# Kernel tuning notes

Hardware: AMD Instinct MI355X
Metric: run time of the kernel (lower is better)

The kernel has to match this reference:

```python
import jax, jax.numpy as jnp
import numpy as np

N_NODES = 50000
N_EDGES = 800000
IN_DIM = 128
HID = 64
HEADS = 4
OUT_DIM = 128
NEG_SLOPE = 0.2


def setup_inputs() -> dict:
    key = jax.random.key(0)
    ks = jax.random.split(key, 11)
    x = jax.random.normal(ks[0], (N_NODES, IN_DIM), dtype=jnp.float32)
    edge_index = jax.random.randint(ks[1], (2, N_EDGES), 0, N_NODES, dtype=jnp.int64)
    s1 = 1.0 / np.sqrt(IN_DIM)
    s2 = 1.0 / np.sqrt(HEADS * HID)
    W1 = jax.random.normal(ks[2], (IN_DIM, HEADS * HID), dtype=jnp.float32) * s1
    a_src1 = jax.random.normal(ks[3], (HEADS, HID), dtype=jnp.float32) * s2
    a_dst1 = jax.random.normal(ks[4], (HEADS, HID), dtype=jnp.float32) * s2
    b1 = jnp.zeros((HEADS * HID,), dtype=jnp.float32)
    W2 = jax.random.normal(ks[5], (HEADS * HID, OUT_DIM), dtype=jnp.float32) * s2
    a_src2 = jax.random.normal(ks[6], (1, OUT_DIM), dtype=jnp.float32) * 0.1
    a_dst2 = jax.random.normal(ks[7], (1, OUT_DIM), dtype=jnp.float32) * 0.1
    b2 = jnp.zeros((OUT_DIM,), dtype=jnp.float32)
    return {"x": x, "edge_index": edge_index, "W1": W1, "a_src1": a_src1,
            "a_dst1": a_dst1, "b1": b1, "W2": W2, "a_src2": a_src2,
            "a_dst2": a_dst2, "b2": b2}


def _gat_conv(x, src, dst, W, a_src, a_dst, bias, heads, out_per_head, concat):
    n = x.shape[0]
    # linear projection per head: [N, H, F]
    h = (x @ W).reshape(n, heads, out_per_head)
    # per-node attention terms: [N, H]
    alpha_src = jnp.einsum('nhf,hf->nh', h, a_src)
    alpha_dst = jnp.einsum('nhf,hf->nh', h, a_dst)
    # edge logits with LeakyReLU: [E, H]
    e = jax.nn.leaky_relu(alpha_src[src] + alpha_dst[dst], NEG_SLOPE)
    # softmax over incoming edges of each destination node
    m = jax.ops.segment_max(e, dst, num_segments=n)  # [N, H]
    m = jnp.where(jnp.isfinite(m), m, 0.0)
    e = jnp.exp(e - m[dst])
    denom = jax.ops.segment_sum(e, dst, num_segments=n)  # [N, H]
    alpha = e / (denom[dst] + 1e-16)  # [E, H]
    # weighted scatter-aggregate of source messages
    out = jax.ops.segment_sum(h[src] * alpha[:, :, None], dst, num_segments=n)  # [N, H, F]
    if concat:
        out = out.reshape(n, heads * out_per_head)
    else:
        out = out.mean(axis=1)
    return out + bias


def reference(x, edge_index, W1, a_src1, a_dst1, b1, W2, a_src2, a_dst2, b2):
    n = x.shape[0]
    # PyG GATConv adds self-loops by default
    loops = jnp.arange(n, dtype=edge_index.dtype)
    src = jnp.concatenate([edge_index[0], loops])
    dst = jnp.concatenate([edge_index[1], loops])
    # dropout layers are identity in inference
    h = _gat_conv(x, src, dst, W1, a_src1, a_dst1, b1, HEADS, HID, True)
    h = jax.nn.elu(h)
    out = _gat_conv(h, src, dst, W2, a_src2, a_dst2, b2, 1, OUT_DIM, True)
    # F.normalize(p=2, dim=1)
    norm = jnp.linalg.norm(out, axis=1, keepdims=True)
    return out / jnp.maximum(norm, 1e-12)
```

## Files before the change

### kernel.cpp

```cpp
#include <hip/hip_runtime.h>
#include <hip/hip_fp16.h>
#include <math.h>

#define N_NODES 50000
#define N_EDGES 800000
#define ET (N_EDGES + N_NODES)
#define IN_DIM 128
#define HID 64
#define HEADS 4
#define C1 (HEADS * HID)
#define OUT_DIM 128
#define NEG_SLOPE 0.2f
#define MTILES 3125
#define G1GRP 782
#define SCB 977
#define SCAN_B 1024
#define NSCB 49
#define HB 64
#define EPB (N_EDGES / HB)

typedef _Float16 h8 __attribute__((ext_vector_type(8)));
typedef float f4 __attribute__((ext_vector_type(4)));
typedef unsigned short u16;

__device__ __forceinline__ float leaky(float v) { return fmaxf(v, NEG_SLOPE * v); }
__device__ __forceinline__ float elu(float v) { return v > 0.0f ? v : expm1f(v); }

__device__ __forceinline__ void fma_mix8(float* acc, h8 v, float w) {
    union { h8 h; int i[4]; } u; u.h = v;
#pragma unroll
    for (int k = 0; k < 4; ++k) {
        asm("v_fma_mix_f32 %0, %1, %2, %0 op_sel:[0,0,0] op_sel_hi:[1,0,0]"
            : "+v"(acc[2 * k]) : "v"(u.i[k]), "v"(w));
        asm("v_fma_mix_f32 %0, %1, %2, %0 op_sel:[1,0,0] op_sel_hi:[1,0,0]"
            : "+v"(acc[2 * k + 1]) : "v"(u.i[k]), "v"(w));
    }
}

__global__ __launch_bounds__(256) void hist_kernel(
        const float* __restrict__ W1, const float* __restrict__ W2,
        __half* __restrict__ w1t, __half* __restrict__ w2t,
        const int* __restrict__ dst, u16* __restrict__ cnt_mat,
        u16* __restrict__ lrank16) {
    __shared__ unsigned pk[N_NODES / 4];
    const int b = blockIdx.x, t = threadIdx.x;
    for (int i = b * 256 + t; i < IN_DIM * C1; i += HB * 256) {
        int k1 = i >> 8, n1 = i & 255;
        w1t[n1 * IN_DIM + k1] = __float2half(W1[i]);
        int k2 = i >> 7, n2 = i & 127;
        w2t[n2 * C1 + k2] = __float2half(W2[i]);
    }
    const int e0 = b * EPB;
    const int4* d4p = (const int4*)(dst + e0);
#pragma unroll
    for (int half = 0; half < 2; ++half) {
        const int nbase = half * (N_NODES / 2);
        for (int i = t; i < N_NODES / 4; i += 256) pk[i] = 0;
        __syncthreads();
        for (int k4 = t; k4 < EPB / 4; k4 += 256) {
            int4 d4 = d4p[k4];
            int dd0 = d4.x - nbase, dd1 = d4.y - nbase;
            int dd2 = d4.z - nbase, dd3 = d4.w - nbase;
            if ((unsigned)dd0 < (unsigned)(N_NODES / 2)) {
                unsigned r = atomicAdd(&pk[dd0 >> 1], (dd0 & 1) ? 65536u : 1u);
                lrank16[e0 + k4 * 4 + 0] = (u16)((dd0 & 1) ? (r >> 16) : (r & 0xffffu));
            }
            if ((unsigned)dd1 < (unsigned)(N_NODES / 2)) {
                unsigned r = atomicAdd(&pk[dd1 >> 1], (dd1 & 1) ? 65536u : 1u);
                lrank16[e0 + k4 * 4 + 1] = (u16)((dd1 & 1) ? (r >> 16) : (r & 0xffffu));
            }
            if ((unsigned)dd2 < (unsigned)(N_NODES / 2)) {
                unsigned r = atomicAdd(&pk[dd2 >> 1], (dd2 & 1) ? 65536u : 1u);
                lrank16[e0 + k4 * 4 + 2] = (u16)((dd2 & 1) ? (r >> 16) : (r & 0xffffu));
            }
            if ((unsigned)dd3 < (unsigned)(N_NODES / 2)) {
                unsigned r = atomicAdd(&pk[dd3 >> 1], (dd3 & 1) ? 65536u : 1u);
                lrank16[e0 + k4 * 4 + 3] = (u16)((dd3 & 1) ? (r >> 16) : (r & 0xffffu));
            }
        }
        __syncthreads();
        unsigned* crow = (unsigned*)(cnt_mat + (size_t)b * N_NODES) + half * (N_NODES / 4);
        for (int i = t; i < N_NODES / 4; i += 256) crow[i] = pk[i];
        __syncthreads();
    }
}

__global__ void scan_local(const u16* __restrict__ cnt_mat, u16* __restrict__ boff,
                           int* __restrict__ lscan, int* __restrict__ bsum) {
    __shared__ int wsum[16];
    const int t = threadIdx.x, lane = t & 63, wv = t >> 6;
    int idx = blockIdx.x * SCAN_B + t;
    int run = 0;
    if (idx < N_NODES) {
#pragma unroll 8
        for (int b = 0; b < HB; ++b) {
            u16 c = cnt_mat[(size_t)b * N_NODES + idx];
            boff[(size_t)b * N_NODES + idx] = (u16)run;
            run += c;
        }
    }
    int v = (idx < N_NODES) ? run + 1 : 0;
    int sc = v;
#pragma unroll
    for (int o = 1; o < 64; o <<= 1) {
        int u = __shfl_up(sc, o);
        if (lane >= o) sc += u;
    }
    if (lane == 63) wsum[wv] = sc;
    __syncthreads();
    if (t == 0) {
        int run2 = 0;
#pragma unroll
        for (int w = 0; w < 16; ++w) { int s = wsum[w]; wsum[w] = run2; run2 += s; }
        bsum[blockIdx.x] = run2;
    }
    __syncthreads();
    if (idx < N_NODES) lscan[idx] = sc + wsum[wv];
}

__global__ void scan_final(const int* __restrict__ lscan, const int* __restrict__ bsum,
                           int* __restrict__ rp) {
    __shared__ int base;
    if (threadIdx.x == 0) {
        int s = 0;
        for (int b = 0; b < blockIdx.x; ++b) s += bsum[b];
        base = s;
    }
    __syncthreads();
    int idx = blockIdx.x * SCAN_B + threadIdx.x;
    if (idx == 0) rp[0] = 0;
    if (idx >= N_NODES) return;
    rp[idx + 1] = lscan[idx] + base;
}

__global__ __launch_bounds__(256) void gemm1_scatter(
        const float* __restrict__ x, const __half* __restrict__ w1t,
        const float* __restrict__ aws, const float* __restrict__ awd,
        __half* __restrict__ hpm, float* __restrict__ as1m, float* __restrict__ ad1m,
        const int* __restrict__ src, const int* __restrict__ dst,
        const u16* __restrict__ lrank16, const u16* __restrict__ boff,
        const int* __restrict__ rp, u16* __restrict__ cs16) {
    const int q9 = blockIdx.x / 9, r9 = blockIdx.x % 9;
    if (r9 >= 4) {
        int si = q9 * 5 + (r9 - 4);
        int tid = si * 256 + threadIdx.x;
        if (tid < N_EDGES / 4) {
            const int b = tid / (EPB / 4);
            const u16* bo = boff + (size_t)b * N_NODES;
            int4 s4 = ((const int4*)src)[tid];
            int4 d4 = ((const int4*)dst)[tid];
            ushort4 r4 = ((const ushort4*)lrank16)[tid];
            cs16[rp[d4.x] + (int)bo[d4.x] + (int)r4.x] = (u16)s4.x;
            cs16[rp[d4.y] + (int)bo[d4.y] + (int)r4.y] = (u16)s4.y;
            cs16[rp[d4.z] + (int)bo[d4.z] + (int)r4.z] = (u16)s4.z;
            cs16[rp[d4.w] + (int)bo[d4.w] + (int)r4.w] = (u16)s4.w;
        } else {
            int d = tid - N_EDGES / 4;
            if (d < N_NODES) cs16[rp[d + 1] - 1] = (u16)d;
        }
        return;
    }
    const int g = q9 * 4 + r9;
    const int tile = g * 4 + (threadIdx.x >> 6);
    if (tile >= MTILES) return;
    const int lane = threadIdx.x & 63;
    const int m0 = tile * 16, lm = lane & 15, lq = lane >> 4;
    h8 afrag[4];
    const float4* xrow = (const float4*)(x + (size_t)(m0 + lm) * IN_DIM + lq * 8);
#pragma unroll
    for (int kt = 0; kt < 4; ++kt) {
        float4 a = xrow[kt * 8];
        float4 b = xrow[kt * 8 + 1];
        union { h8 v; __half2 p[4]; } u;
        u.p[0] = __floats2half2_rn(a.x, a.y);
        u.p[1] = __floats2half2_rn(a.z, a.w);
        u.p[2] = __floats2half2_rn(b.x, b.y);
        u.p[3] = __floats2half2_rn(b.z, b.w);
        afrag[kt] = u.v;
    }
    f4 acc[16];
#pragma unroll
    for (int nt = 0; nt < 16; ++nt) acc[nt] = (f4){0.f, 0.f, 0.f, 0.f};
#pragma unroll
    for (int nt = 0; nt < 16; ++nt) {
        const h8* brow = (const h8*)(w1t + (size_t)(nt * 16 + lm) * IN_DIM + lq * 8);
#pragma unroll
        for (int kt = 0; kt < 4; ++kt)
            acc[nt] = __builtin_amdgcn_mfma_f32_16x16x32_f16(afrag[kt], brow[kt * 4],
                                                             acc[nt], 0, 0, 0);
    }
    float sS[4][4] = {{0.f}}, sD[4][4] = {{0.f}};
#pragma unroll
    for (int nt = 0; nt < 16; ++nt) {
        int col = nt * 16 + lm;
        float wa = aws[col], wd = awd[col];
        int hd = nt >> 2;
        int pr = nt >> 3;
        int cip = col & 127;
#pragma unroll
        for (int r = 0; r < 4; ++r) {
            float v = acc[nt][r];
            hpm[((size_t)pr * N_NODES + (m0 + lq * 4 + r)) * 128 + cip] = __float2half(v);
            sS[hd][r] += v * wa;
            sD[hd][r] += v * wd;
        }
    }
#pragma unroll
    for (int o = 1; o < 16; o <<= 1) {
#pragma unroll
        for (int hd = 0; hd < 4; ++hd)
#pragma unroll
            for (int r = 0; r < 4; ++r) {
                sS[hd][r] += __shfl_xor(sS[hd][r], o);
                sD[hd][r] += __shfl_xor(sD[hd][r], o);
            }
    }
    if (lm == 0) {
        float2* asp = (float2*)as1m;
        float2* adp = (float2*)ad1m;
#pragma unroll
        for (int r = 0; r < 4; ++r) {
            int row = m0 + lq * 4 + r;
            asp[row]           = make_float2(sS[0][r], sS[1][r]);
            asp[N_NODES + row] = make_float2(sS[2][r], sS[3][r]);
            adp[row]           = make_float2(sD[0][r], sD[1][r]);
            adp[N_NODES + row] = make_float2(sD[2][r], sD[3][r]);
        }
    }
}

__global__ __launch_bounds__(256) void gemm2_mfma(
        const __half* __restrict__ ah, const __half* __restrict__ w2t,
        const float* __restrict__ aws, const float* __restrict__ awd,
        __half* __restrict__ h, float* __restrict__ as2, float* __restrict__ ad2) {
    const int tile = blockIdx.x * 4 + (threadIdx.x >> 6);
    if (tile >= MTILES) return;
    const int lane = threadIdx.x & 63;
    const int m0 = tile * 16, lm = lane & 15, lq = lane >> 4;
    h8 afrag[8];
    const h8* arow = (const h8*)(ah + (size_t)(m0 + lm) * C1 + lq * 8);
#pragma unroll
    for (int kt = 0; kt < 8; ++kt) afrag[kt] = arow[kt * 4];
    f4 acc[8];
#pragma unroll
    for (int nt = 0; nt < 8; ++nt) acc[nt] = (f4){0.f, 0.f, 0.f, 0.f};
#pragma unroll
    for (int nt = 0; nt < 8; ++nt) {
        const h8* brow = (const h8*)(w2t + (size_t)(nt * 16 + lm) * C1 + lq * 8);
#pragma unroll
        for (int kt = 0; kt < 8; ++kt)
            acc[nt] = __builtin_amdgcn_mfma_f32_16x16x32_f16(afrag[kt], brow[kt * 4],
                                                             acc[nt], 0, 0, 0);
    }
    float sS[4] = {0.f, 0.f, 0.f, 0.f}, sD[4] = {0.f, 0.f, 0.f, 0.f};
#pragma unroll
    for (int nt = 0; nt < 8; ++nt) {
        int col = nt * 16 + lm;
        float wa = aws[col], wd = awd[col];
#pragma unroll
        for (int r = 0; r < 4; ++r) {
            float v = acc[nt][r];
            h[(size_t)(m0 + lq * 4 + r) * OUT_DIM + col] = __float2half(v);
            sS[r] += v * wa;
            sD[r] += v * wd;
        }
    }
#pragma unroll
    for (int o = 1; o < 16; o <<= 1) {
#pragma unroll
        for (int r = 0; r < 4; ++r) {
            sS[r] += __shfl_xor(sS[r], o);
            sD[r] += __shfl_xor(sD[r], o);
        }
    }
    if (lm == 0) {
#pragma unroll
        for (int r = 0; r < 4; ++r) {
            int row = m0 + lq * 4 + r;
            as2[row] = sS[r];
            ad2[row] = sD[r];
        }
    }
}

__global__ __launch_bounds__(256) void aggregate1_fused(
        const int* __restrict__ rp, const u16* __restrict__ cs16,
        const __half* __restrict__ hpm, const float* __restrict__ as1m,
        const float* __restrict__ ad1m, const float* __restrict__ b1,
        __half* __restrict__ out1h) {
    __shared__ int4 stg[8][32];
    const int pair = blockIdx.x & 1, g = blockIdx.x >> 1;
    const int hw = threadIdx.x >> 5, li = threadIdx.x & 31;
    const int d = g * 8 + hw;
    const int e0 = rp[d], deg = rp[d + 1] - e0;
    const float2* asb = (const float2*)as1m + (size_t)pair * N_NODES;
    const float2 adv = ((const float2*)ad1m)[(size_t)pair * N_NODES + d];
    const char* hb = (const char*)hpm + (size_t)pair * N_NODES * 256;
    const int es = li >> 4, fl = li & 15;
    const int hip = fl >> 3;
    const int lbyte = fl * 16;
    float acc[8] = {0.f, 0.f, 0.f, 0.f, 0.f, 0.f, 0.f, 0.f};
    float ds0 = 0.f, ds1 = 0.f;
    for (int c0 = 0; c0 < deg; c0 += 32) {
        const int clen = min(32, deg - c0);
        int idx = c0 + li;
        bool valid = idx < deg;
        int s = valid ? (int)cs16[e0 + idx] : 0;
        float2 av = asb[s];
        float x0 = valid ? __expf(leaky(av.x + adv.x)) : 0.f;
        float x1 = valid ? __expf(leaky(av.y + adv.y)) : 0.f;
        stg[hw][li] = make_int4(s << 8, __float_as_int(x0), __float_as_int(x1), 0);
        ds0 += x0; ds1 += x1;
        __builtin_amdgcn_wave_barrier();
        int j = 0;
        for (; j + 8 <= clen; j += 8) {
            int4 p0 = stg[hw][j + es];
            int4 p1 = stg[hw][j + 2 + es];
            int4 p2 = stg[hw][j + 4 + es];
            int4 p3 = stg[hw][j + 6 + es];
            h8 v0 = *(const h8*)(hb + p0.x + lbyte);
            h8 v1 = *(const h8*)(hb + p1.x + lbyte);
            h8 v2 = *(const h8*)(hb + p2.x + lbyte);
            h8 v3 = *(const h8*)(hb + p3.x + lbyte);
            fma_mix8(acc, v0, __int_as_float(hip ? p0.z : p0.y));
            fma_mix8(acc, v1, __int_as_float(hip ? p1.z : p1.y));
            fma_mix8(acc, v2, __int_as_float(hip ? p2.z : p2.y));
            fma_mix8(acc, v3, __int_as_float(hip ? p3.z : p3.y));
        }
        for (; j < clen; j += 2) {
            int4 p0 = stg[hw][j + es];
            h8 v0 = *(const h8*)(hb + p0.x + lbyte);
            fma_mix8(acc, v0, __int_as_float(hip ? p0.z : p0.y));
        }
        __builtin_amdgcn_wave_barrier();
    }
#pragma unroll
    for (int f = 0; f < 8; ++f) acc[f] += __shfl_xor(acc[f], 16);
#pragma unroll
    for (int o = 16; o > 0; o >>= 1) {
        ds0 += __shfl_xor(ds0, o);
        ds1 += __shfl_xor(ds1, o);
    }
    if (es == 0) {
        float den = hip ? ds1 : ds0;
        float inv = 1.0f / (den + 1e-16f);
        float4 bA = ((const float4*)b1)[pair * 32 + fl * 2];
        float4 bB = ((const float4*)b1)[pair * 32 + fl * 2 + 1];
        h8 o;
        o[0] = (_Float16)elu(acc[0] * inv + bA.x);
        o[1] = (_Float16)elu(acc[1] * inv + bA.y);
        o[2] = (_Float16)elu(acc[2] * inv + bA.z);
        o[3] = (_Float16)elu(acc[3] * inv + bA.w);
        o[4] = (_Float16)elu(acc[4] * inv + bB.x);
        o[5] = (_Float16)elu(acc[5] * inv + bB.y);
        o[6] = (_Float16)elu(acc[6] * inv + bB.z);
        o[7] = (_Float16)elu(acc[7] * inv + bB.w);
        *(h8*)((char*)out1h + (size_t)d * 512 + pair * 256 + lbyte) = o;
    }
}

__global__ __launch_bounds__(256) void aggregate2_fused(
        const int* __restrict__ rp, const u16* __restrict__ cs16,
        const __half* __restrict__ h2h, const float* __restrict__ as2,
        const float* __restrict__ ad2, const float* __restrict__ b2,
        float* __restrict__ out) {
    __shared__ int2 stg[8][32];
    const int hw = threadIdx.x >> 5, li = threadIdx.x & 31;
    const int d = blockIdx.x * 8 + hw;
    const int e0 = rp[d], deg = rp[d + 1] - e0;
    const float adv = ad2[d];
    const int q = li >> 4, lo = li & 15;
    const int lbyte = lo * 16;
    const char* hbase = (const char*)h2h;
    float acc[8] = {0.f, 0.f, 0.f, 0.f, 0.f, 0.f, 0.f, 0.f};
    float dsum = 0.f;
    for (int c0 = 0; c0 < deg; c0 += 32) {
        const int clen = min(32, deg - c0);
        int idx = c0 + li;
        bool valid = idx < deg;
        int s = valid ? (int)cs16[e0 + idx] : 0;
        float xv = valid ? __expf(leaky(as2[s] + adv)) : 0.f;
        stg[hw][li] = make_int2(s << 8, __float_as_int(xv));
        dsum += xv;
        __builtin_amdgcn_wave_barrier();
        int j = 0;
        for (; j + 8 <= clen; j += 8) {
            int2 p0 = stg[hw][j + q];
            int2 p1 = stg[hw][j + 2 + q];
            int2 p2 = stg[hw][j + 4 + q];
            int2 p3 = stg[hw][j + 6 + q];
            h8 v0 = *(const h8*)(hbase + p0.x + lbyte);
            h8 v1 = *(const h8*)(hbase + p1.x + lbyte);
            h8 v2 = *(const h8*)(hbase + p2.x + lbyte);
            h8 v3 = *(const h8*)(hbase + p3.x + lbyte);
            fma_mix8(acc, v0, __int_as_float(p0.y));
            fma_mix8(acc, v1, __int_as_float(p1.y));
            fma_mix8(acc, v2, __int_as_float(p2.y));
            fma_mix8(acc, v3, __int_as_float(p3.y));
        }
        for (; j < clen; j += 2) {
            int2 p0 = stg[hw][j + q];
            h8 v0 = *(const h8*)(hbase + p0.x + lbyte);
            fma_mix8(acc, v0, __int_as_float(p0.y));
        }
        __builtin_amdgcn_wave_barrier();
    }
#pragma unroll
    for (int f = 0; f < 8; ++f) acc[f] += __shfl_xor(acc[f], 16);
#pragma unroll
    for (int o = 16; o > 0; o >>= 1) dsum += __shfl_xor(dsum, o);
    if (q == 0) {
        float inv = 1.0f / (dsum + 1e-16f);
        float4 bA = ((const float4*)b2)[lo * 2];
        float4 bB = ((const float4*)b2)[lo * 2 + 1];
        float v0 = acc[0] * inv + bA.x, v1 = acc[1] * inv + bA.y;
        float v2 = acc[2] * inv + bA.z, v3 = acc[3] * inv + bA.w;
        float v4 = acc[4] * inv + bB.x, v5 = acc[5] * inv + bB.y;
        float v6 = acc[6] * inv + bB.z, v7 = acc[7] * inv + bB.w;
        float ss = v0 * v0 + v1 * v1 + v2 * v2 + v3 * v3 +
                   v4 * v4 + v5 * v5 + v6 * v6 + v7 * v7;
#pragma unroll
        for (int o = 1; o < 16; o <<= 1) ss += __shfl_xor(ss, o);
        float sc = 1.0f / fmaxf(sqrtf(ss), 1e-12f);
        float4* orow = (float4*)((char*)out + (size_t)d * 512 + lo * 32);
        orow[0] = make_float4(v0 * sc, v1 * sc, v2 * sc, v3 * sc);
        orow[1] = make_float4(v4 * sc, v5 * sc, v6 * sc, v7 * sc);
    }
}

extern "C" void kernel_launch(void* const* d_in, const int* in_sizes, int n_in,
                              void* d_out, int out_size, void* d_ws, size_t ws_size,
                              hipStream_t stream) {
    const float* x     = (const float*)d_in[0];
    const int*   edge  = (const int*)d_in[1];
    const int*   src   = edge;
    const int*   dst   = edge + N_EDGES;
    const float* W1    = (const float*)d_in[2];
    const float* aw_s1 = (const float*)d_in[3];
    const float* aw_d1 = (const float*)d_in[4];
    const float* b1    = (const float*)d_in[5];
    const float* W2    = (const float*)d_in[6];
    const float* aw_s2 = (const float*)d_in[7];
    const float* aw_d2 = (const float*)d_in[8];
    const float* b2    = (const float*)d_in[9];
    float* out = (float*)d_out;

    char* ws = (char*)d_ws;
    size_t off = 0;
    auto alloc = [&](size_t bytes) {
        void* p = ws + off;
        off += (bytes + 255) & ~(size_t)255;
        return p;
    };
    u16*    cs16    = (u16*)alloc((size_t)ET * 2);
    u16*    lrank16 = (u16*)alloc((size_t)N_EDGES * 2);
    u16*    cnt_mat = (u16*)alloc((size_t)HB * N_NODES * 2);
    u16*    boff    = (u16*)alloc((size_t)HB * N_NODES * 2);
    int*    rp      = (int*)alloc((size_t)(N_NODES + 1) * 4);
    int*    lscan   = (int*)alloc((size_t)NSCB * SCAN_B * 4);
    int*    bsum    = (int*)alloc((size_t)NSCB * 4);
    float*  as1     = (float*)alloc((size_t)N_NODES * HEADS * 4);
    float*  ad1     = (float*)alloc((size_t)N_NODES * HEADS * 4);
    float*  as2     = (float*)alloc((size_t)N_NODES * 4);
    float*  ad2     = (float*)alloc((size_t)N_NODES * 4);
    __half* w1t     = (__half*)alloc((size_t)IN_DIM * C1 * 2);
    __half* w2t     = (__half*)alloc((size_t)C1 * OUT_DIM * 2);
    __half* hpm     = (__half*)alloc((size_t)N_NODES * C1 * 2);
    __half* out1h   = (__half*)alloc((size_t)N_NODES * C1 * 2);
    __half* h2h     = hpm;
    (void)off;


    hist_kernel<<<HB, 256, 0, stream>>>(W1, W2, w1t, w2t, dst, cnt_mat, lrank16);
    scan_local<<<NSCB, SCAN_B, 0, stream>>>(cnt_mat, boff, lscan, bsum);
    scan_final<<<NSCB, SCAN_B, 0, stream>>>(lscan, bsum, rp);
    gemm1_scatter<<<196 * 9, 256, 0, stream>>>(x, w1t, aw_s1, aw_d1, hpm, as1, ad1,
                                               src, dst, lrank16, boff, rp, cs16);

    aggregate1_fused<<<(N_NODES / 8) * 2, 256, 0, stream>>>(rp, cs16, hpm, as1, ad1, b1, out1h);

    gemm2_mfma<<<(MTILES + 3) / 4, 256, 0, stream>>>(out1h, w2t, aw_s2, aw_d2, h2h, as2, ad2);
    aggregate2_fused<<<N_NODES / 8, 256, 0, stream>>>(rp, cs16, h2h, as2, ad2, b2, out);
}
```

Baseline: 295.8 us.

## Split histogram into quarter-node blocks and split two big launches in half

The histogram kernel now runs 256 blocks, each covering one quarter of the node range, instead of 64 blocks that each loop over two halves. Each block uses a smaller shared array and needs fewer syncs, and the weight conversion loop becomes a single strided pass. The gemm1_scatter and aggregate1_fused launches are each split into two launches with a block-offset parameter. Every block still reads its full edge slice, so total dst reads per block-set grow fourfold, and the extra launches add overhead.

```diff
diff --git a/kernel.cpp b/kernel.cpp
--- a/kernel.cpp
+++ b/kernel.cpp
@@ -13,11 +13,11 @@
 #define NEG_SLOPE 0.2f
 #define MTILES 3125
 #define G1GRP 782
-#define SCB 977
 #define SCAN_B 1024
 #define NSCB 49
 #define HB 64
 #define EPB (N_EDGES / HB)
+#define NQ (N_NODES / 4)
 
 typedef _Float16 h8 __attribute__((ext_vector_type(8)));
 typedef float f4 __attribute__((ext_vector_type(4)));
@@ -42,47 +42,48 @@
         __half* __restrict__ w1t, __half* __restrict__ w2t,
         const int* __restrict__ dst, u16* __restrict__ cnt_mat,
         u16* __restrict__ lrank16) {
-    __shared__ unsigned pk[N_NODES / 4];
-    const int b = blockIdx.x, t = threadIdx.x;
-    for (int i = b * 256 + t; i < IN_DIM * C1; i += HB * 256) {
-        int k1 = i >> 8, n1 = i & 255;
-        w1t[n1 * IN_DIM + k1] = __float2half(W1[i]);
-        int k2 = i >> 7, n2 = i & 127;
-        w2t[n2 * C1 + k2] = __float2half(W2[i]);
+    __shared__ unsigned pk[NQ / 2];
+    const int b = blockIdx.x >> 2;
+    const int qd = blockIdx.x & 3;
+    const int t = threadIdx.x;
+    {
+        int i = blockIdx.x * 256 + t;
+        if (i < IN_DIM * C1) {
+            int k1 = i >> 8, n1 = i & 255;
+            w1t[n1 * IN_DIM + k1] = __float2half(W1[i]);
+            int k2 = i >> 7, n2 = i & 127;
+            w2t[n2 * C1 + k2] = __float2half(W2[i]);
+        }
     }
     const int e0 = b * EPB;
+    const int nbase = qd * NQ;
+    for (int i = t; i < NQ / 2; i += 256) pk[i] = 0;
+    __syncthreads();
     const int4* d4p = (const int4*)(dst + e0);
-#pragma unroll
-    for (int half = 0; half < 2; ++half) {
-        const int nbase = half * (N_NODES / 2);
-        for (int i = t; i < N_NODES / 4; i += 256) pk[i] = 0;
-        __syncthreads();
-        for (int k4 = t; k4 < EPB / 4; k4 += 256) {
-            int4 d4 = d4p[k4];
-            int dd0 = d4.x - nbase, dd1 = d4.y - nbase;
-            int dd2 = d4.z - nbase, dd3 = d4.w - nbase;
-            if ((unsigned)dd0 < (unsigned)(N_NODES / 2)) {
-                unsigned r = atomicAdd(&pk[dd0 >> 1], (dd0 & 1) ? 65536u : 1u);
-                lrank16[e0 + k4 * 4 + 0] = (u16)((dd0 & 1) ? (r >> 16) : (r & 0xffffu));
-            }
-            if ((unsigned)dd1 < (unsigned)(N_NODES / 2)) {
-                unsigned r = atomicAdd(&pk[dd1 >> 1], (dd1 & 1) ? 65536u : 1u);
-                lrank16[e0 + k4 * 4 + 1] = (u16)((dd1 & 1) ? (r >> 16) : (r & 0xffffu));
-            }
-            if ((unsigned)dd2 < (unsigned)(N_NODES / 2)) {
-                unsigned r = atomicAdd(&pk[dd2 >> 1], (dd2 & 1) ? 65536u : 1u);
-                lrank16[e0 + k4 * 4 + 2] = (u16)((dd2 & 1) ? (r >> 16) : (r & 0xffffu));
-            }
-            if ((unsigned)dd3 < (unsigned)(N_NODES / 2)) {
-                unsigned r = atomicAdd(&pk[dd3 >> 1], (dd3 & 1) ? 65536u : 1u);
-                lrank16[e0 + k4 * 4 + 3] = (u16)((dd3 & 1) ? (r >> 16) : (r & 0xffffu));
-            }
-        }
-        __syncthreads();
-        unsigned* crow = (unsigned*)(cnt_mat + (size_t)b * N_NODES) + half * (N_NODES / 4);
-        for (int i = t; i < N_NODES / 4; i += 256) crow[i] = pk[i];
-        __syncthreads();
-    }
+    for (int k4 = t; k4 < EPB / 4; k4 += 256) {
+        int4 d4 = d4p[k4];
+        int dd0 = d4.x - nbase, dd1 = d4.y - nbase;
+        int dd2 = d4.z - nbase, dd3 = d4.w - nbase;
+        if ((unsigned)dd0 < (unsigned)NQ) {
+            unsigned r = atomicAdd(&pk[dd0 >> 1], (dd0 & 1) ? 65536u : 1u);
+            lrank16[e0 + k4 * 4 + 0] = (u16)((dd0 & 1) ? (r >> 16) : (r & 0xffffu));
+        }
+        if ((unsigned)dd1 < (unsigned)NQ) {
+            unsigned r = atomicAdd(&pk[dd1 >> 1], (dd1 & 1) ? 65536u : 1u);
+            lrank16[e0 + k4 * 4 + 1] = (u16)((dd1 & 1) ? (r >> 16) : (r & 0xffffu));
+        }
+        if ((unsigned)dd2 < (unsigned)NQ) {
+            unsigned r = atomicAdd(&pk[dd2 >> 1], (dd2 & 1) ? 65536u : 1u);
+            lrank16[e0 + k4 * 4 + 2] = (u16)((dd2 & 1) ? (r >> 16) : (r & 0xffffu));
+        }
+        if ((unsigned)dd3 < (unsigned)NQ) {
+            unsigned r = atomicAdd(&pk[dd3 >> 1], (dd3 & 1) ? 65536u : 1u);
+            lrank16[e0 + k4 * 4 + 3] = (u16)((dd3 & 1) ? (r >> 16) : (r & 0xffffu));
+        }
+    }
+    __syncthreads();
+    unsigned* crow = (unsigned*)(cnt_mat + (size_t)b * N_NODES + nbase);
+    for (int i = t; i < NQ / 2; i += 256) crow[i] = pk[i];
 }
 
 __global__ void scan_local(const u16* __restrict__ cnt_mat, u16* __restrict__ boff,
@@ -139,8 +140,9 @@
         __half* __restrict__ hpm, float* __restrict__ as1m, float* __restrict__ ad1m,
         const int* __restrict__ src, const int* __restrict__ dst,
         const u16* __restrict__ lrank16, const u16* __restrict__ boff,
-        const int* __restrict__ rp, u16* __restrict__ cs16) {
-    const int q9 = blockIdx.x / 9, r9 = blockIdx.x % 9;
+        const int* __restrict__ rp, u16* __restrict__ cs16, int gbase) {
+    const int vb = blockIdx.x + gbase;
+    const int q9 = vb / 9, r9 = vb % 9;
     if (r9 >= 4) {
         int si = q9 * 5 + (r9 - 4);
         int tid = si * 256 + threadIdx.x;
@@ -287,9 +289,10 @@
         const int* __restrict__ rp, const u16* __restrict__ cs16,
         const __half* __restrict__ hpm, const float* __restrict__ as1m,
         const float* __restrict__ ad1m, const float* __restrict__ b1,
-        __half* __restrict__ out1h) {
+        __half* __restrict__ out1h, int gbase) {
     __shared__ int4 stg[8][32];
-    const int pair = blockIdx.x & 1, g = blockIdx.x >> 1;
+    const int vb = blockIdx.x + gbase;
+    const int pair = vb & 1, g = vb >> 1;
     const int hw = threadIdx.x >> 5, li = threadIdx.x & 31;
     const int d = g * 8 + hw;
     const int e0 = rp[d], deg = rp[d + 1] - e0;
@@ -471,13 +474,16 @@
     (void)off;
 
 
-    hist_kernel<<<HB, 256, 0, stream>>>(W1, W2, w1t, w2t, dst, cnt_mat, lrank16);
+    hist_kernel<<<HB * 4, 256, 0, stream>>>(W1, W2, w1t, w2t, dst, cnt_mat, lrank16);
     scan_local<<<NSCB, SCAN_B, 0, stream>>>(cnt_mat, boff, lscan, bsum);
     scan_final<<<NSCB, SCAN_B, 0, stream>>>(lscan, bsum, rp);
-    gemm1_scatter<<<196 * 9, 256, 0, stream>>>(x, w1t, aw_s1, aw_d1, hpm, as1, ad1,
-                                               src, dst, lrank16, boff, rp, cs16);
-
-    aggregate1_fused<<<(N_NODES / 8) * 2, 256, 0, stream>>>(rp, cs16, hpm, as1, ad1, b1, out1h);
+    gemm1_scatter<<<882, 256, 0, stream>>>(x, w1t, aw_s1, aw_d1, hpm, as1, ad1,
+                                           src, dst, lrank16, boff, rp, cs16, 0);
+    gemm1_scatter<<<882, 256, 0, stream>>>(x, w1t, aw_s1, aw_d1, hpm, as1, ad1,
+                                           src, dst, lrank16, boff, rp, cs16, 882);
+
+    aggregate1_fused<<<6250, 256, 0, stream>>>(rp, cs16, hpm, as1, ad1, b1, out1h, 0);
+    aggregate1_fused<<<6250, 256, 0, stream>>>(rp, cs16, hpm, as1, ad1, b1, out1h, 6250);
 
     gemm2_mfma<<<(MTILES + 3) / 4, 256, 0, stream>>>(out1h, w2t, aw_s2, aw_d2, h2h, as2, ad2);
     aggregate2_fused<<<N_NODES / 8, 256, 0, stream>>>(rp, cs16, h2h, as2, ad2, b2, out);
```

Result: slower. 303.0 us (+2.5%).
